# Performance work log

Hardware: AMD Instinct MI355X
Metric: run time of the kernel (lower is better)

## Reference

```python
import jax, jax.numpy as jnp
import numpy as np

B, N, K, U = 64, 4096, 32, 16
NUM_STEPS = 8
NUM_CLASSES = 2


def setup_inputs() -> dict:
    key = jax.random.key(0)
    ks = jax.random.split(key, 17)
    s = 0.05
    g = lambda k, shape: jax.random.normal(k, shape, dtype=jnp.float32) * s
    return {
        "inputs": jax.random.normal(ks[0], (B, N, K + 2), dtype=jnp.float32),
        # UGRNN cell params
        "Wn": g(ks[1], (K, U)),
        "Wg": g(ks[2], (U, U)), "Ug": g(ks[3], (U, U)), "bg": jnp.zeros((U,), jnp.float32),
        "Wc": g(ks[4], (U, U)), "Uc": g(ks[5], (U, U)), "bc": jnp.zeros((U,), jnp.float32),
        "We": g(ks[6], (U, U)), "be": jnp.zeros((U,), jnp.float32),
        # MLP head (Dropout is identity at inference)
        "W1": g(ks[7], (N * U, 256)), "b1": jnp.zeros((256,), jnp.float32),
        "W2": g(ks[8], (256, 32)),    "b2": jnp.zeros((32,), jnp.float32),
        "W3": g(ks[9], (32, NUM_CLASSES)), "b3": jnp.zeros((NUM_CLASSES,), jnp.float32),
    }


def reference(inputs, Wn, Wg, Ug, bg, Wc, Uc, bc, We, be, W1, b1, W2, b2, W3, b3):
    # split channels: node scalar, K neighbour features, edge scalar
    h0 = inputs[..., 0]            # [B, N]
    neigh = inputs[..., 1:-1]      # [B, N, K]
    e0 = inputs[..., -1]           # [B, N]

    units = Wg.shape[0]
    h = jnp.broadcast_to(h0[..., None], h0.shape + (units,))  # tile -> [B, N, U]
    e = jnp.broadcast_to(e0[..., None], e0.shape + (units,))  # tile -> [B, N, U]

    # neighbour aggregation/projection is constant across steps -> hoist
    m = jnp.einsum("bnk,ku->bnu", neigh, Wn)  # [B, N, U]

    for _ in range(NUM_STEPS):  # small fixed unroll over num_steps
        x = m + e
        g = jax.nn.sigmoid(x @ Wg + h @ Ug + bg)  # update gate
        c = jnp.tanh(x @ Wc + h @ Uc + bc)        # candidate
        h = g * h + (1.0 - g) * c                 # UGRNN update
        e = jnp.tanh(x @ We + be)                 # edge state update

    out = h.reshape(h.shape[0], -1)               # Flatten -> [B, N*U]
    out = jax.nn.relu(out @ W1 + b1)
    out = jax.nn.relu(out @ W2 + b2)
    return jax.nn.softmax(out @ W3 + b3, axis=-1)  # [B, num_classes]
```

## Files before the change

kernel.cpp:

```cpp
#include <hip/hip_runtime.h>
#include <hip/hip_bf16.h>

typedef _Float16 half8_t __attribute__((ext_vector_type(8)));
typedef _Float16 half4_t __attribute__((ext_vector_type(4)));
typedef float    f32x4  __attribute__((ext_vector_type(4)));

#define MFMA16(a, b, c) __builtin_amdgcn_mfma_f32_16x16x32_f16((a), (b), (c), 0, 0, 0)

__device__ __forceinline__ void load_lds16(const void* g, void* l) {
    __builtin_amdgcn_global_load_lds(
        (const __attribute__((address_space(1))) unsigned int*)g,
        (__attribute__((address_space(3))) unsigned int*)l, 16, 0, 0);
}

__global__
__attribute__((amdgpu_flat_work_group_size(256, 256), amdgpu_waves_per_eu(1, 3)))
void ugrnn_mfma(
    const float* __restrict__ inputs,
    const float* __restrict__ Wn, const float* __restrict__ Wg,
    const float* __restrict__ Ug, const float* __restrict__ bg,
    const float* __restrict__ Wc, const float* __restrict__ Uc,
    const float* __restrict__ bc, const float* __restrict__ We,
    const float* __restrict__ be, _Float16* __restrict__ h_t)
{
    __shared__ float     raw[4][2 * 544];
    __shared__ _Float16  T[4][2][32][20];

    const int wave = threadIdx.x >> 6;
    const int lane = threadIdx.x & 63;
    const int t16  = lane & 15;
    const int q    = lane >> 4;

    const int pair = blockIdx.x * 4 + wave;
    const int b    = pair >> 7;
    const int n0   = (pair & 127) << 5;

    const float* gsrc = inputs + ((size_t)b * 4096 + n0) * 34;
    float* rw = raw[wave];
#pragma unroll
    for (int r = 0; r < 17; ++r) rw[r * 64 + lane] = gsrc[r * 64 + lane];

    half8_t Bn, Bg8, Bc8, Be8;
#pragma unroll
    for (int i = 0; i < 8; ++i) {
        int kk = q * 8 + i;
        Bn[i] = (_Float16)Wn[kk * 16 + t16];
        float gv = (kk < 16) ? Wg[kk * 16 + t16] : Ug[(kk - 16) * 16 + t16];
        float cv = (kk < 16) ? Wc[kk * 16 + t16] : Uc[(kk - 16) * 16 + t16];
        float ev = (kk < 16) ? We[kk * 16 + t16] : 0.0f;
        Bg8[i] = (_Float16)gv;
        Bc8[i] = (_Float16)cv;
        Be8[i] = (_Float16)ev;
    }
    float bgv = bg[t16], bcv = bc[t16], bev = be[t16];
    f32x4 bgC = {bgv, bgv, bgv, bgv};
    f32x4 bcC = {bcv, bcv, bcv, bcv};
    f32x4 beC = {bev, bev, bev, bev};

    asm volatile("s_waitcnt lgkmcnt(0)" ::: "memory");

    f32x4 m[2], h[2], e[2];
    f32x4 zc = {0.f, 0.f, 0.f, 0.f};
#pragma unroll
    for (int u2 = 0; u2 < 2; ++u2) {
        const float* rt = rw + u2 * 544;
        half8_t An;
#pragma unroll
        for (int i = 0; i < 8; ++i)
            An[i] = (_Float16)rt[t16 * 34 + 1 + q * 8 + i];
        m[u2] = MFMA16(An, Bn, zc);
#pragma unroll
        for (int r = 0; r < 4; ++r) {
            h[u2][r] = rt[(4 * q + r) * 34 + 0];
            e[u2][r] = rt[(4 * q + r) * 34 + 33];
        }
    }

#pragma unroll 1
    for (int step = 0; step < 8; ++step) {
#pragma unroll
        for (int u2 = 0; u2 < 2; ++u2) {
            f32x4 x = m[u2] + e[u2];
            half4_t xp, hp;
#pragma unroll
            for (int r = 0; r < 4; ++r) { xp[r] = (_Float16)x[r]; hp[r] = (_Float16)h[u2][r]; }
            _Float16* Tw = &T[wave][u2][0][0];
            *(half4_t*)&Tw[t16 * 20 + 4 * q]        = xp;
            *(half4_t*)&Tw[(16 + t16) * 20 + 4 * q] = hp;
        }
        asm volatile("s_waitcnt lgkmcnt(0)" ::: "memory");

        f32x4 gp[2], cp[2], ep[2];
#pragma unroll
        for (int u2 = 0; u2 < 2; ++u2) {
            const _Float16* Tw = &T[wave][u2][0][0];
            half8_t A;
#pragma unroll
            for (int i = 0; i < 8; ++i)
                A[i] = Tw[(q * 8 + i) * 20 + t16];
            gp[u2] = MFMA16(A, Bg8, bgC);
            cp[u2] = MFMA16(A, Bc8, bcC);
            if (step < 7) ep[u2] = MFMA16(A, Be8, beC);
        }

#pragma unroll
        for (int u2 = 0; u2 < 2; ++u2) {
#pragma unroll
            for (int r = 0; r < 4; ++r) {
                float gv = __builtin_amdgcn_rcpf(1.0f + __expf(-gp[u2][r]));
                float cv = 1.0f - 2.0f * __builtin_amdgcn_rcpf(1.0f + __expf(2.0f * cp[u2][r]));
                h[u2][r] = cv + gv * (h[u2][r] - cv);
                if (step < 7)
                    e[u2][r] = 1.0f - 2.0f * __builtin_amdgcn_rcpf(1.0f + __expf(2.0f * ep[u2][r]));
            }
        }
    }

    _Float16* hd = h_t + (size_t)b * 65536 + (size_t)n0 * 16 + t16;
#pragma unroll
    for (int u2 = 0; u2 < 2; ++u2)
#pragma unroll
        for (int r = 0; r < 4; ++r)
            hd[(u2 * 16 + 4 * q + r) * 16] = (_Float16)h[u2][r];
}

__global__
__attribute__((amdgpu_flat_work_group_size(256, 256), amdgpu_waves_per_eu(1, 2)))
void fc1_mfma(const _Float16* __restrict__ h_t, const float* __restrict__ W1,
              _Float16* __restrict__ partials)
{
    __shared__ float w1s[2][64][258];
    const int tid  = threadIdx.x;
    const int wave = tid >> 6;
    const int lane = tid & 63;
    const int t16  = lane & 15;
    const int q    = lane >> 4;
    const int i0   = blockIdx.x * 256;

    f32x4 acc[4][4];
#pragma unroll
    for (int mt = 0; mt < 4; ++mt)
#pragma unroll
        for (int nt = 0; nt < 4; ++nt)
            acc[mt][nt] = (f32x4){0.f, 0.f, 0.f, 0.f};

#pragma unroll
    for (int r = 0; r < 16; ++r) {
        int row = wave * 16 + r;
        load_lds16(W1 + (size_t)(i0 + row) * 256 + lane * 4, &w1s[0][row][0]);
    }
    __syncthreads();

#pragma unroll 1
    for (int c = 0; c < 4; ++c) {
        const int buf = c & 1;
        const int cb  = i0 + c * 64;

        half8_t A[2][4];
#pragma unroll
        for (int ks = 0; ks < 2; ++ks)
#pragma unroll
            for (int mt = 0; mt < 4; ++mt)
                A[ks][mt] = *(const half8_t*)(h_t
                    + (size_t)(mt * 16 + t16) * 65536 + cb + ks * 32 + q * 8);

        if (c < 3) {
#pragma unroll
            for (int r = 0; r < 16; ++r) {
                int row = wave * 16 + r;
                load_lds16(W1 + (size_t)(cb + 64 + row) * 256 + lane * 4,
                           &w1s[buf ^ 1][row][0]);
            }
        }

#pragma unroll
        for (int ks = 0; ks < 2; ++ks) {
#pragma unroll
            for (int nt = 0; nt < 4; ++nt) {
                int j = (wave * 4 + nt) * 16 + t16;
                half8_t Bf;
#pragma unroll
                for (int i = 0; i < 8; ++i)
                    Bf[i] = (_Float16)w1s[buf][ks * 32 + q * 8 + i][j];
#pragma unroll
                for (int mt = 0; mt < 4; ++mt)
                    acc[mt][nt] = MFMA16(A[ks][mt], Bf, acc[mt][nt]);
            }
        }
        __syncthreads();
    }

    _Float16* pb = partials + (size_t)blockIdx.x * 16384;
#pragma unroll
    for (int mt = 0; mt < 4; ++mt)
#pragma unroll
        for (int nt = 0; nt < 4; ++nt)
#pragma unroll
            for (int r = 0; r < 4; ++r)
                pb[(mt * 16 + 4 * q + r) * 256 + (wave * 4 + nt) * 16 + t16] =
                    (_Float16)acc[mt][nt][r];
}

__global__ __launch_bounds__(256) void mlp_tail(
    const _Float16* __restrict__ partials, const float* __restrict__ b1,
    const float* __restrict__ W2, const float* __restrict__ b2,
    const float* __restrict__ W3, const float* __restrict__ b3,
    float* __restrict__ out)
{
    __shared__ float x1[256];
    __shared__ float x2[32];
    __shared__ float lg[2];
    const int b = blockIdx.x, j = threadIdx.x;

    const _Float16* p = partials + (size_t)b * 256 + j;
    float s0 = 0.f, s1 = 0.f, s2 = 0.f, s3 = 0.f;
#pragma unroll 8
    for (int k = 0; k < 256; k += 4) {
        s0 += (float)p[(size_t)(k + 0) * 16384];
        s1 += (float)p[(size_t)(k + 1) * 16384];
        s2 += (float)p[(size_t)(k + 2) * 16384];
        s3 += (float)p[(size_t)(k + 3) * 16384];
    }
    x1[j] = fmaxf(b1[j] + s0 + s1 + s2 + s3, 0.0f);
    __syncthreads();

    if (j < 32) {
        float s = b2[j];
#pragma unroll 8
        for (int k = 0; k < 256; ++k) s += x1[k] * W2[k * 32 + j];
        x2[j] = fmaxf(s, 0.0f);
    }
    __syncthreads();

    if (j < 2) {
        float s = b3[j];
#pragma unroll
        for (int k = 0; k < 32; ++k) s += x2[k] * W3[k * 2 + j];
        lg[j] = s;
    }
    __syncthreads();

    if (j == 0) {
        float mx = fmaxf(lg[0], lg[1]);
        float e0 = __expf(lg[0] - mx), e1 = __expf(lg[1] - mx);
        float inv = 1.0f / (e0 + e1);
        out[b * 2 + 0] = e0 * inv;
        out[b * 2 + 1] = e1 * inv;
    }
}

extern "C" void kernel_launch(void* const* d_in, const int* in_sizes, int n_in,
                              void* d_out, int out_size, void* d_ws, size_t ws_size,
                              hipStream_t stream) {
    const float* inputs = (const float*)d_in[0];
    const float* Wn = (const float*)d_in[1];
    const float* Wg = (const float*)d_in[2];
    const float* Ug = (const float*)d_in[3];
    const float* bg = (const float*)d_in[4];
    const float* Wc = (const float*)d_in[5];
    const float* Uc = (const float*)d_in[6];
    const float* bc = (const float*)d_in[7];
    const float* We = (const float*)d_in[8];
    const float* be = (const float*)d_in[9];
    const float* W1 = (const float*)d_in[10];
    const float* b1 = (const float*)d_in[11];
    const float* W2 = (const float*)d_in[12];
    const float* b2 = (const float*)d_in[13];
    const float* W3 = (const float*)d_in[14];
    const float* b3 = (const float*)d_in[15];
    float* out = (float*)d_out;

    _Float16* h_t      = (_Float16*)d_ws;
    _Float16* partials = (_Float16*)((char*)d_ws + (size_t)64 * 65536 * 2);

    ugrnn_mfma<<<2048, 256, 0, stream>>>(inputs, Wn, Wg, Ug, bg, Wc, Uc, bc,
                                         We, be, h_t);
    fc1_mfma<<<256, 256, 0, stream>>>(h_t, W1, partials);
    mlp_tail<<<64, 256, 0, stream>>>(partials, b1, W2, b2, W3, b3, out);
}
```

Measured before the change: 215.3 us.

## Transpose UGRNN MFMA orientation to drop LDS round-trip; widen mlp_tail reduction

```diff
diff --git a/kernel.cpp b/kernel.cpp
--- a/kernel.cpp
+++ b/kernel.cpp
@@ -5,7 +5,8 @@
 typedef _Float16 half4_t __attribute__((ext_vector_type(4)));
 typedef float    f32x4  __attribute__((ext_vector_type(4)));
 
-#define MFMA16(a, b, c) __builtin_amdgcn_mfma_f32_16x16x32_f16((a), (b), (c), 0, 0, 0)
+#define MFMA32(a, b, c) __builtin_amdgcn_mfma_f32_16x16x32_f16((a), (b), (c), 0, 0, 0)
+#define MFMA16(a, b, c) __builtin_amdgcn_mfma_f32_16x16x16f16((a), (b), (c), 0, 0, 0)
 
 __device__ __forceinline__ void load_lds16(const void* g, void* l) {
     __builtin_amdgcn_global_load_lds(
@@ -14,7 +15,7 @@
 }
 
 __global__
-__attribute__((amdgpu_flat_work_group_size(256, 256), amdgpu_waves_per_eu(1, 3)))
+__attribute__((amdgpu_flat_work_group_size(256, 256)))
 void ugrnn_mfma(
     const float* __restrict__ inputs,
     const float* __restrict__ Wn, const float* __restrict__ Wg,
@@ -23,8 +24,7 @@
     const float* __restrict__ bc, const float* __restrict__ We,
     const float* __restrict__ be, _Float16* __restrict__ h_t)
 {
-    __shared__ float     raw[4][2 * 544];
-    __shared__ _Float16  T[4][2][32][20];
+    __shared__ float raw[4][2 * 544];
 
     const int wave = threadIdx.x >> 6;
     const int lane = threadIdx.x & 63;
@@ -40,69 +40,61 @@
 #pragma unroll
     for (int r = 0; r < 17; ++r) rw[r * 64 + lane] = gsrc[r * 64 + lane];
 
-    half8_t Bn, Bg8, Bc8, Be8;
-#pragma unroll
-    for (int i = 0; i < 8; ++i) {
-        int kk = q * 8 + i;
-        Bn[i] = (_Float16)Wn[kk * 16 + t16];
-        float gv = (kk < 16) ? Wg[kk * 16 + t16] : Ug[(kk - 16) * 16 + t16];
-        float cv = (kk < 16) ? Wc[kk * 16 + t16] : Uc[(kk - 16) * 16 + t16];
-        float ev = (kk < 16) ? We[kk * 16 + t16] : 0.0f;
-        Bg8[i] = (_Float16)gv;
-        Bc8[i] = (_Float16)cv;
-        Be8[i] = (_Float16)ev;
-    }
-    float bgv = bg[t16], bcv = bc[t16], bev = be[t16];
-    f32x4 bgC = {bgv, bgv, bgv, bgv};
-    f32x4 bcC = {bcv, bcv, bcv, bcv};
-    f32x4 beC = {bev, bev, bev, bev};
-
-    asm volatile("s_waitcnt lgkmcnt(0)" ::: "memory");
+    half8_t An;
+#pragma unroll
+    for (int i = 0; i < 8; ++i)
+        An[i] = (_Float16)Wn[(q * 8 + i) * 16 + t16];
+
+    half4_t Awg, Aug, Awc, Auc, Awe;
+#pragma unroll
+    for (int i = 0; i < 4; ++i) {
+        const int k = 4 * q + i;
+        Awg[i] = (_Float16)Wg[k * 16 + t16];
+        Aug[i] = (_Float16)Ug[k * 16 + t16];
+        Awc[i] = (_Float16)Wc[k * 16 + t16];
+        Auc[i] = (_Float16)Uc[k * 16 + t16];
+        Awe[i] = (_Float16)We[k * 16 + t16];
+    }
+    f32x4 bgC, bcC, beC;
+#pragma unroll
+    for (int r = 0; r < 4; ++r) {
+        bgC[r] = bg[4 * q + r];
+        bcC[r] = bc[4 * q + r];
+        beC[r] = be[4 * q + r];
+    }
 
     f32x4 m[2], h[2], e[2];
-    f32x4 zc = {0.f, 0.f, 0.f, 0.f};
+    const f32x4 zc = {0.f, 0.f, 0.f, 0.f};
 #pragma unroll
     for (int u2 = 0; u2 < 2; ++u2) {
         const float* rt = rw + u2 * 544;
-        half8_t An;
+        half8_t Bx;
 #pragma unroll
         for (int i = 0; i < 8; ++i)
-            An[i] = (_Float16)rt[t16 * 34 + 1 + q * 8 + i];
-        m[u2] = MFMA16(An, Bn, zc);
-#pragma unroll
-        for (int r = 0; r < 4; ++r) {
-            h[u2][r] = rt[(4 * q + r) * 34 + 0];
-            e[u2][r] = rt[(4 * q + r) * 34 + 33];
-        }
+            Bx[i] = (_Float16)rt[t16 * 34 + 1 + q * 8 + i];
+        m[u2] = MFMA32(An, Bx, zc);
+        const float h0 = rt[t16 * 34 + 0];
+        const float e0 = rt[t16 * 34 + 33];
+        h[u2] = (f32x4){h0, h0, h0, h0};
+        e[u2] = (f32x4){e0, e0, e0, e0};
     }
 
 #pragma unroll 1
     for (int step = 0; step < 8; ++step) {
+        f32x4 gp[2], cp[2], ep[2];
 #pragma unroll
         for (int u2 = 0; u2 < 2; ++u2) {
-            f32x4 x = m[u2] + e[u2];
-            half4_t xp, hp;
-#pragma unroll
-            for (int r = 0; r < 4; ++r) { xp[r] = (_Float16)x[r]; hp[r] = (_Float16)h[u2][r]; }
-            _Float16* Tw = &T[wave][u2][0][0];
-            *(half4_t*)&Tw[t16 * 20 + 4 * q]        = xp;
-            *(half4_t*)&Tw[(16 + t16) * 20 + 4 * q] = hp;
-        }
-        asm volatile("s_waitcnt lgkmcnt(0)" ::: "memory");
-
-        f32x4 gp[2], cp[2], ep[2];
-#pragma unroll
-        for (int u2 = 0; u2 < 2; ++u2) {
-            const _Float16* Tw = &T[wave][u2][0][0];
-            half8_t A;
-#pragma unroll
-            for (int i = 0; i < 8; ++i)
-                A[i] = Tw[(q * 8 + i) * 20 + t16];
-            gp[u2] = MFMA16(A, Bg8, bgC);
-            cp[u2] = MFMA16(A, Bc8, bcC);
-            if (step < 7) ep[u2] = MFMA16(A, Be8, beC);
-        }
-
+            const f32x4 x = m[u2] + e[u2];
+            half4_t xB, hB;
+#pragma unroll
+            for (int r = 0; r < 4; ++r) {
+                xB[r] = (_Float16)x[r];
+                hB[r] = (_Float16)h[u2][r];
+            }
+            gp[u2] = MFMA16(Aug, hB, MFMA16(Awg, xB, bgC));
+            cp[u2] = MFMA16(Auc, hB, MFMA16(Awc, xB, bcC));
+            if (step < 7) ep[u2] = MFMA16(Awe, xB, beC);
+        }
 #pragma unroll
         for (int u2 = 0; u2 < 2; ++u2) {
 #pragma unroll
@@ -116,12 +108,14 @@
         }
     }
 
-    _Float16* hd = h_t + (size_t)b * 65536 + (size_t)n0 * 16 + t16;
-#pragma unroll
-    for (int u2 = 0; u2 < 2; ++u2)
-#pragma unroll
-        for (int r = 0; r < 4; ++r)
-            hd[(u2 * 16 + 4 * q + r) * 16] = (_Float16)h[u2][r];
+#pragma unroll
+    for (int u2 = 0; u2 < 2; ++u2) {
+        half4_t hv;
+#pragma unroll
+        for (int r = 0; r < 4; ++r) hv[r] = (_Float16)h[u2][r];
+        *(half4_t*)(h_t + (size_t)b * 65536
+                        + (size_t)(n0 + u2 * 16 + t16) * 16 + 4 * q) = hv;
+    }
 }
 
 __global__
@@ -184,7 +178,7 @@
                     Bf[i] = (_Float16)w1s[buf][ks * 32 + q * 8 + i][j];
 #pragma unroll
                 for (int mt = 0; mt < 4; ++mt)
-                    acc[mt][nt] = MFMA16(A[ks][mt], Bf, acc[mt][nt]);
+                    acc[mt][nt] = MFMA32(A[ks][mt], Bf, acc[mt][nt]);
             }
         }
         __syncthreads();
@@ -201,46 +195,56 @@
                     (_Float16)acc[mt][nt][r];
 }
 
-__global__ __launch_bounds__(256) void mlp_tail(
+__global__ __launch_bounds__(1024) void mlp_tail(
     const _Float16* __restrict__ partials, const float* __restrict__ b1,
     const float* __restrict__ W2, const float* __restrict__ b2,
     const float* __restrict__ W3, const float* __restrict__ b3,
     float* __restrict__ out)
 {
-    __shared__ float x1[256];
-    __shared__ float x2[32];
+    __shared__ float x1p[4][256];
+    __shared__ float x1s[256];
+    __shared__ float x2q[32][33];
+    __shared__ float x2s[32];
     __shared__ float lg[2];
-    const int b = blockIdx.x, j = threadIdx.x;
-
-    const _Float16* p = partials + (size_t)b * 256 + j;
+    const int b = blockIdx.x, tid = threadIdx.x;
+    const int j = tid & 255, kg = tid >> 8;
+
+    const _Float16* p = partials + (size_t)(kg * 64) * 16384 + (size_t)b * 256 + j;
     float s0 = 0.f, s1 = 0.f, s2 = 0.f, s3 = 0.f;
-#pragma unroll 8
-    for (int k = 0; k < 256; k += 4) {
+#pragma unroll 4
+    for (int k = 0; k < 64; k += 4) {
         s0 += (float)p[(size_t)(k + 0) * 16384];
         s1 += (float)p[(size_t)(k + 1) * 16384];
         s2 += (float)p[(size_t)(k + 2) * 16384];
         s3 += (float)p[(size_t)(k + 3) * 16384];
     }
-    x1[j] = fmaxf(b1[j] + s0 + s1 + s2 + s3, 0.0f);
-    __syncthreads();
-
-    if (j < 32) {
-        float s = b2[j];
-#pragma unroll 8
-        for (int k = 0; k < 256; ++k) s += x1[k] * W2[k * 32 + j];
-        x2[j] = fmaxf(s, 0.0f);
-    }
-    __syncthreads();
-
-    if (j < 2) {
-        float s = b3[j];
-#pragma unroll
-        for (int k = 0; k < 32; ++k) s += x2[k] * W3[k * 2 + j];
-        lg[j] = s;
-    }
-    __syncthreads();
-
-    if (j == 0) {
+    x1p[kg][j] = s0 + s1 + s2 + s3;
+    __syncthreads();
+    if (tid < 256)
+        x1s[j] = fmaxf(b1[j] + x1p[0][j] + x1p[1][j] + x1p[2][j] + x1p[3][j], 0.f);
+    __syncthreads();
+
+    const int j2 = tid & 31, g2 = tid >> 5;
+    float s = 0.f;
+#pragma unroll
+    for (int k = g2 * 8; k < g2 * 8 + 8; ++k) s += x1s[k] * W2[k * 32 + j2];
+    x2q[g2][j2] = s;
+    __syncthreads();
+    if (tid < 32) {
+        float t = b2[tid];
+#pragma unroll
+        for (int g = 0; g < 32; ++g) t += x2q[g][tid];
+        x2s[tid] = fmaxf(t, 0.f);
+    }
+    __syncthreads();
+    if (tid < 2) {
+        float t = b3[tid];
+#pragma unroll
+        for (int k = 0; k < 32; ++k) t += x2s[k] * W3[k * 2 + tid];
+        lg[tid] = t;
+    }
+    __syncthreads();
+    if (tid == 0) {
         float mx = fmaxf(lg[0], lg[1]);
         float e0 = __expf(lg[0] - mx), e1 = __expf(lg[1] - mx);
         float inv = 1.0f / (e0 + e1);
@@ -276,5 +280,5 @@
     ugrnn_mfma<<<2048, 256, 0, stream>>>(inputs, Wn, Wg, Ug, bg, Wc, Uc, bc,
                                          We, be, h_t);
     fc1_mfma<<<256, 256, 0, stream>>>(h_t, W1, partials);
-    mlp_tail<<<64, 256, 0, stream>>>(partials, b1, W2, b2, W3, b3, out);
-}
+    mlp_tail<<<64, 1024, 0, stream>>>(partials, b1, W2, b2, W3, b3, out);
+}
```

After: 182.9 us. -15.1%, faster.
